# Optimization experiments

Measured on AMD Instinct MI355X. Metric: run time of the kernel, lower is better.

## Reference

```python
import jax, jax.numpy as jnp
import numpy as np

N = 100000
E = 1000000
H = 128
DF = 64
TOTAL_GENES = 20000
NUM_PERTS = 5000


def setup_inputs() -> dict:
    key = jax.random.key(0)
    ks = jax.random.split(key, 32)
    d_in1 = DF + H  # all_feat=True: concat raw feats with gene embedding

    def g(k, shape, scale=0.05):
        return jax.random.normal(k, shape, dtype=jnp.float32) * scale

    inp = {
        'x': jax.random.normal(ks[0], (N, DF), dtype=jnp.float32),
        'edge_index': jax.random.randint(ks[1], (2, E), 0, N),
        'edge_attr': jax.random.normal(ks[2], (E, 1), dtype=jnp.float32),
        'pert': jax.random.randint(ks[3], (N,), 0, NUM_PERTS),
        'ctrl': jax.random.normal(ks[4], (N, 1), dtype=jnp.float32),
        'pos': jax.random.randint(ks[5], (N,), 0, TOTAL_GENES),
        # learned parameters
        'gene_table': g(ks[6], (TOTAL_GENES, H), 1.0),
        'pert_table': g(ks[7], (NUM_PERTS, H), 1.0),
        'W1': g(ks[8], (d_in1, H)), 'a_src1': g(ks[9], (H,)), 'a_dst1': g(ks[10], (H,)), 'b1': g(ks[11], (H,)),
        'Wl1': g(ks[12], (d_in1, H)), 'bl1': g(ks[13], (H,)),
        'W2': g(ks[14], (H, H)), 'a_src2': g(ks[15], (H,)), 'a_dst2': g(ks[16], (H,)), 'b2': g(ks[17], (H,)),
        'Wl2': g(ks[18], (H, H)), 'bl2': g(ks[19], (H,)),
        'Wm1': g(ks[20], (2 * H + 1, H // 2)), 'bm1': g(ks[21], (H // 2,)),
        'Wm2': g(ks[22], (H // 2, 1)), 'bm2': g(ks[23], (1,)),
    }
    return inp


def gat_conv(x, src, dst, W, a_src, a_dst, b, n_nodes):
    # PyG GATConv, heads=1, concat=False, negative_slope=0.2, add_self_loops
    h = x @ W                         # [N, H]
    asrc = h @ a_src                  # [N]
    adst = h @ a_dst                  # [N]
    loop = jnp.arange(n_nodes)
    s = jnp.concatenate([src, loop])  # [E+N]
    d = jnp.concatenate([dst, loop])
    e = jax.nn.leaky_relu(asrc[s] + adst[d], negative_slope=0.2)
    m = jax.ops.segment_max(e, d, num_segments=n_nodes)
    ex = jnp.exp(e - m[d])
    denom = jax.ops.segment_sum(ex, d, num_segments=n_nodes)
    alpha = ex / (denom[d] + 1e-16)
    out = jax.ops.segment_sum(h[s] * alpha[:, None], d, num_segments=n_nodes)
    return out + b


def _forward(x, edge_attr, ctrl, gene_table, pert_table,
             W1, a_src1, a_dst1, b1, Wl1, bl1,
             W2, a_src2, a_dst2, b2, Wl2, bl2,
             Wm1, bm1, Wm2, bm2,
             edge_index, pert, pos):
    src, dst = edge_index[0], edge_index[1]
    # gene embedding with max_norm=True (rows renormed to norm <= 1.0)
    pe = gene_table[pos]
    nrm = jnp.linalg.norm(pe, axis=-1, keepdims=True)
    pe = jnp.where(nrm > 1.0, pe / (nrm + 1e-7), pe)
    h = jnp.concatenate([x, pe], axis=1)            # [N, DF+H]
    h = gat_conv(h, src, dst, W1, a_src1, a_dst1, b1, x.shape[0]) + h @ Wl1 + bl1
    h = jax.nn.relu(h)
    h = gat_conv(h, src, dst, W2, a_src2, a_dst2, b2, x.shape[0]) + h @ Wl2 + bl2
    z = jnp.concatenate([h, ctrl, pert_table[pert]], axis=1)  # [N, 2H+1]
    z = jax.nn.relu(z @ Wm1 + bm1)
    z = jax.nn.relu(z @ Wm2 + bm2)
    return z.squeeze(1)


def reference(x, edge_index, edge_attr, pert, ctrl, pos,
              gene_table, pert_table,
              W1, a_src1, a_dst1, b1, Wl1, bl1,
              W2, a_src2, a_dst2, b2, Wl2, bl2,
              Wm1, bm1, Wm2, bm2):
    return _forward(x, edge_attr, ctrl, gene_table, pert_table,
                    W1, a_src1, a_dst1, b1, Wl1, bl1,
                    W2, a_src2, a_dst2, b2, Wl2, bl2,
                    Wm1, bm1, Wm2, bm2,
                    edge_index, pert, pos)
```

## Files before the change

### kernel.cpp

```cpp
#include <hip/hip_runtime.h>
#include <hip/hip_bf16.h>

typedef __bf16 bf16;
typedef __bf16 bf16x8 __attribute__((ext_vector_type(8)));
typedef __bf16 bf16x4 __attribute__((ext_vector_type(4)));
typedef __bf16 bf16x2 __attribute__((ext_vector_type(2)));
typedef float f32x4 __attribute__((ext_vector_type(4)));

#define CAP 48

__device__ __forceinline__ float b2f(bf16 v) { return (float)v; }
__device__ __forceinline__ bf16 f2b(float v) { return (bf16)v; }

__device__ __forceinline__ float leaky(float x) { return fmaxf(x, 0.2f * x); }

__device__ __forceinline__ bf16x8 zero8() {
    bf16x8 v;
    #pragma unroll
    for (int j = 0; j < 8; ++j) v[j] = (bf16)0.0f;
    return v;
}

__device__ __forceinline__ void swizzle_one(const float* __restrict__ W, bf16* __restrict__ dst,
                                            int f, int NT, int Kreal, int C) {
    int kb = f / (NT * 64);
    int rem = f % (NT * 64);
    int nt = rem / 64;
    int ln = rem % 64;
    int q = ln >> 4, m = ln & 15;
    int c = nt * 16 + m;
    bf16x8 v;
    #pragma unroll
    for (int j = 0; j < 8; ++j) {
        int k = kb * 32 + q * 8 + j;
        v[j] = (k < Kreal) ? f2b(W[k * C + c]) : (bf16)0.0f;
    }
    *reinterpret_cast<bf16x8*>(dst + f * 8) = v;
}

__global__ void scatter_kernel(const int* __restrict__ e_src, const int* __restrict__ e_dst,
                               int* __restrict__ cnt, int* __restrict__ colidx, int e,
                               const float* __restrict__ W1, const float* __restrict__ Wl1,
                               const float* __restrict__ W2, const float* __restrict__ Wl2,
                               const float* __restrict__ Wm1,
                               bf16* __restrict__ w1s, bf16* __restrict__ wl1s,
                               bf16* __restrict__ w2s, bf16* __restrict__ wl2s,
                               bf16* __restrict__ wm1s) {
    int bid = blockIdx.x;
    if (bid < 49) {
        int g = bid * blockDim.x + threadIdx.x;
        if (g < 3072)        swizzle_one(W1,  w1s,  g,          8, 192, 128);
        else if (g < 6144)   swizzle_one(Wl1, wl1s, g - 3072,   8, 192, 128);
        else if (g < 8192)   swizzle_one(W2,  w2s,  g - 6144,   8, 128, 128);
        else if (g < 10240)  swizzle_one(Wl2, wl2s, g - 8192,   8, 128, 128);
        else if (g < 12544)  swizzle_one(Wm1, wm1s, g - 10240,  4, 257,  64);
        return;
    }
    int i = (bid - 49) * blockDim.x + threadIdx.x;
    if (i < e) {
        int d = __builtin_nontemporal_load(e_dst + i);
        int s = __builtin_nontemporal_load(e_src + i);
        int k = atomicAdd(&cnt[d], 1);
        if (k < CAP) __builtin_nontemporal_store(s, colidx + d * CAP + k);
    }
}

template <int KB>
__global__ __launch_bounds__(256) void gemm_l1_kernel(
    const float* __restrict__ x,
    const float* __restrict__ gene_table,
    const int* __restrict__ pos,
    const bf16* __restrict__ Wg, const bf16* __restrict__ Wl,
    const float* __restrict__ bias_l,
    bf16* __restrict__ outg, bf16* __restrict__ outl, int ldo, int nrows,
    const float* __restrict__ attn_s, const float* __restrict__ attn_d,
    float* __restrict__ asrc, float* __restrict__ adst) {
    const int NTT = 8;
    __shared__ bf16 sH[64][200];
    __shared__ float sA[64][2];
    int tid = threadIdx.x;

    {
        int rsub = tid >> 5, l32 = tid & 31;
        #pragma unroll
        for (int rr = 0; rr < 8; ++rr) {
            int rloc = rr * 8 + rsub;
            long long row = (long long)blockIdx.x * 64 + rloc;
            if (row < nrows) {
                const float* g = gene_table + (long long)pos[row] * 128;
                float4 p = reinterpret_cast<const float4*>(g)[l32];
                float ss = p.x * p.x + p.y * p.y + p.z * p.z + p.w * p.w;
                #pragma unroll
                for (int o = 16; o; o >>= 1) ss += __shfl_xor(ss, o, 32);
                float nrm = sqrtf(ss);
                float sc = nrm > 1.0f ? 1.0f / (nrm + 1e-7f) : 1.0f;
                float2 xv = reinterpret_cast<const float2*>(x + row * 64)[l32];
                sH[rloc][2 * l32]     = f2b(xv.x);
                sH[rloc][2 * l32 + 1] = f2b(xv.y);
                sH[rloc][64 + 4 * l32 + 0] = f2b(p.x * sc);
                sH[rloc][64 + 4 * l32 + 1] = f2b(p.y * sc);
                sH[rloc][64 + 4 * l32 + 2] = f2b(p.z * sc);
                sH[rloc][64 + 4 * l32 + 3] = f2b(p.w * sc);
            } else {
                sH[rloc][2 * l32]     = (bf16)0.0f;
                sH[rloc][2 * l32 + 1] = (bf16)0.0f;
                sH[rloc][64 + 4 * l32 + 0] = (bf16)0.0f;
                sH[rloc][64 + 4 * l32 + 1] = (bf16)0.0f;
                sH[rloc][64 + 4 * l32 + 2] = (bf16)0.0f;
                sH[rloc][64 + 4 * l32 + 3] = (bf16)0.0f;
            }
        }
    }
    __syncthreads();

    int wave = tid >> 6, lane = tid & 63;
    int q = lane >> 4, m = lane & 15;
    int nt0 = (wave & 1) * 4;
    int r0loc = (wave >> 1) * 32 + m;
    long long row_base = (long long)blockIdx.x * 64 + (wave >> 1) * 32;
    long long r0 = row_base + m;
    long long r1 = row_base + 16 + m;

    f32x4 accg[2][4], accl[2][4];
    #pragma unroll
    for (int t = 0; t < 2; ++t)
        #pragma unroll
        for (int nt = 0; nt < 4; ++nt) {
            f32x4 z = {0.f, 0.f, 0.f, 0.f};
            accg[t][nt] = z; accl[t][nt] = z;
        }

    #pragma unroll
    for (int kb = 0; kb < KB; ++kb) {
        bf16x8 b0 = *reinterpret_cast<const bf16x8*>(&sH[r0loc][kb * 32 + q * 8]);
        bf16x8 b1 = *reinterpret_cast<const bf16x8*>(&sH[r0loc + 16][kb * 32 + q * 8]);
        #pragma unroll
        for (int nt = 0; nt < 4; ++nt) {
            bf16x8 wg = *reinterpret_cast<const bf16x8*>(Wg + ((kb * NTT + nt0 + nt) * 64 + lane) * 8);
            bf16x8 wl = *reinterpret_cast<const bf16x8*>(Wl + ((kb * NTT + nt0 + nt) * 64 + lane) * 8);
            accg[0][nt] = __builtin_amdgcn_mfma_f32_16x16x32_bf16(wg, b0, accg[0][nt], 0, 0, 0);
            accg[1][nt] = __builtin_amdgcn_mfma_f32_16x16x32_bf16(wg, b1, accg[1][nt], 0, 0, 0);
            accl[0][nt] = __builtin_amdgcn_mfma_f32_16x16x32_bf16(wl, b0, accl[0][nt], 0, 0, 0);
            accl[1][nt] = __builtin_amdgcn_mfma_f32_16x16x32_bf16(wl, b1, accl[1][nt], 0, 0, 0);
        }
    }
    #pragma unroll
    for (int t = 0; t < 2; ++t) {
        long long row = t ? r1 : r0;
        if (row < nrows) {
            #pragma unroll
            for (int nt = 0; nt < 4; ++nt) {
                int c0 = (nt0 + nt) * 16 + q * 4;
                bf16x4 og, ol;
                #pragma unroll
                for (int r = 0; r < 4; ++r) {
                    og[r] = f2b(accg[t][nt][r]);
                    ol[r] = f2b(accl[t][nt][r] + bias_l[c0 + r]);
                }
                *reinterpret_cast<bf16x4*>(outg + row * ldo + c0) = og;
                *reinterpret_cast<bf16x4*>(outl + row * ldo + c0) = ol;
            }
        }
    }
    float svt[2], dvt[2];
    #pragma unroll
    for (int t = 0; t < 2; ++t) {
        float sv = 0.f, dv = 0.f;
        #pragma unroll
        for (int nt = 0; nt < 4; ++nt) {
            int c0 = (nt0 + nt) * 16 + q * 4;
            #pragma unroll
            for (int r = 0; r < 4; ++r) {
                float v = accg[t][nt][r];
                sv = fmaf(v, attn_s[c0 + r], sv);
                dv = fmaf(v, attn_d[c0 + r], dv);
            }
        }
        sv += __shfl_xor(sv, 16); sv += __shfl_xor(sv, 32);
        dv += __shfl_xor(dv, 16); dv += __shfl_xor(dv, 32);
        svt[t] = sv; dvt[t] = dv;
        if ((wave & 1) == 0 && q == 0) {
            int rloc = (wave >> 1) * 32 + t * 16 + m;
            sA[rloc][0] = sv; sA[rloc][1] = dv;
        }
    }
    __syncthreads();
    #pragma unroll
    for (int t = 0; t < 2; ++t) {
        long long row = t ? r1 : r0;
        if ((wave & 1) == 1 && q == 0 && row < nrows) {
            int rloc = (wave >> 1) * 32 + t * 16 + m;
            asrc[row] = svt[t] + sA[rloc][0];
            adst[row] = dvt[t] + sA[rloc][1];
        }
    }
}

template <int KB>
__global__ __launch_bounds__(256) void gemm_dual_kernel(
    const bf16* __restrict__ A, int lda,
    const bf16* __restrict__ Wg, const bf16* __restrict__ Wl,
    const float* __restrict__ bias_l,
    bf16* __restrict__ outg, bf16* __restrict__ outl, int ldo, int nrows,
    const float* __restrict__ attn_s, const float* __restrict__ attn_d,
    float* __restrict__ asrc, float* __restrict__ adst) {
    const int NTT = 8;
    __shared__ float sA[64][2];
    int tid = threadIdx.x;
    int wave = tid >> 6, lane = tid & 63;
    int q = lane >> 4, m = lane & 15;
    int nt0 = (wave & 1) * 4;
    long long row_base = (long long)blockIdx.x * 64 + (wave >> 1) * 32;
    long long r0 = row_base + m;
    long long r1 = row_base + 16 + m;
    bool v0 = r0 < nrows, v1 = r1 < nrows;

    f32x4 accg[2][4], accl[2][4];
    #pragma unroll
    for (int t = 0; t < 2; ++t)
        #pragma unroll
        for (int nt = 0; nt < 4; ++nt) {
            f32x4 z = {0.f, 0.f, 0.f, 0.f};
            accg[t][nt] = z; accl[t][nt] = z;
        }

    bf16x8 b0 = v0 ? *reinterpret_cast<const bf16x8*>(A + r0 * lda + q * 8) : zero8();
    bf16x8 b1 = v1 ? *reinterpret_cast<const bf16x8*>(A + r1 * lda + q * 8) : zero8();
    #pragma unroll
    for (int kb = 0; kb < KB; ++kb) {
        bf16x8 nb0, nb1;
        if (kb + 1 < KB) {
            nb0 = v0 ? *reinterpret_cast<const bf16x8*>(A + r0 * lda + (kb + 1) * 32 + q * 8) : zero8();
            nb1 = v1 ? *reinterpret_cast<const bf16x8*>(A + r1 * lda + (kb + 1) * 32 + q * 8) : zero8();
        }
        #pragma unroll
        for (int nt = 0; nt < 4; ++nt) {
            bf16x8 wg = *reinterpret_cast<const bf16x8*>(Wg + ((kb * NTT + nt0 + nt) * 64 + lane) * 8);
            bf16x8 wl = *reinterpret_cast<const bf16x8*>(Wl + ((kb * NTT + nt0 + nt) * 64 + lane) * 8);
            accg[0][nt] = __builtin_amdgcn_mfma_f32_16x16x32_bf16(wg, b0, accg[0][nt], 0, 0, 0);
            accg[1][nt] = __builtin_amdgcn_mfma_f32_16x16x32_bf16(wg, b1, accg[1][nt], 0, 0, 0);
            accl[0][nt] = __builtin_amdgcn_mfma_f32_16x16x32_bf16(wl, b0, accl[0][nt], 0, 0, 0);
            accl[1][nt] = __builtin_amdgcn_mfma_f32_16x16x32_bf16(wl, b1, accl[1][nt], 0, 0, 0);
        }
        b0 = nb0; b1 = nb1;
    }
    #pragma unroll
    for (int t = 0; t < 2; ++t) {
        long long row = t ? r1 : r0;
        if (row < nrows) {
            #pragma unroll
            for (int nt = 0; nt < 4; ++nt) {
                int c0 = (nt0 + nt) * 16 + q * 4;
                bf16x4 og, ol;
                #pragma unroll
                for (int r = 0; r < 4; ++r) {
                    og[r] = f2b(accg[t][nt][r]);
                    ol[r] = f2b(accl[t][nt][r] + bias_l[c0 + r]);
                }
                *reinterpret_cast<bf16x4*>(outg + row * ldo + c0) = og;
                *reinterpret_cast<bf16x4*>(outl + row * ldo + c0) = ol;
            }
        }
    }
    float svt[2], dvt[2];
    #pragma unroll
    for (int t = 0; t < 2; ++t) {
        float sv = 0.f, dv = 0.f;
        #pragma unroll
        for (int nt = 0; nt < 4; ++nt) {
            int c0 = (nt0 + nt) * 16 + q * 4;
            #pragma unroll
            for (int r = 0; r < 4; ++r) {
                float v = accg[t][nt][r];
                sv = fmaf(v, attn_s[c0 + r], sv);
                dv = fmaf(v, attn_d[c0 + r], dv);
            }
        }
        sv += __shfl_xor(sv, 16); sv += __shfl_xor(sv, 32);
        dv += __shfl_xor(dv, 16); dv += __shfl_xor(dv, 32);
        svt[t] = sv; dvt[t] = dv;
        if ((wave & 1) == 0 && q == 0) {
            int rloc = (wave >> 1) * 32 + t * 16 + m;
            sA[rloc][0] = sv; sA[rloc][1] = dv;
        }
    }
    __syncthreads();
    #pragma unroll
    for (int t = 0; t < 2; ++t) {
        long long row = t ? r1 : r0;
        if ((wave & 1) == 1 && q == 0 && row < nrows) {
            int rloc = (wave >> 1) * 32 + t * 16 + m;
            asrc[row] = svt[t] + sA[rloc][0];
            adst[row] = dvt[t] + sA[rloc][1];
        }
    }
}

template <int KB, int NT>
__global__ __launch_bounds__(256) void gemm_mlp_kernel(
    const bf16* __restrict__ A, int lda,
    const bf16* __restrict__ Wsw,
    const float* __restrict__ bias, int nrows,
    const float* __restrict__ Wm2, const float* __restrict__ bm2,
    float* __restrict__ out_final) {
    int tid = threadIdx.x;
    int wave = tid >> 6, lane = tid & 63;
    int q = lane >> 4, m = lane & 15;
    long long row_base = (long long)blockIdx.x * 128 + wave * 32;
    long long r0 = row_base + m;
    long long r1 = row_base + 16 + m;
    bool v0 = r0 < nrows, v1 = r1 < nrows;

    f32x4 acc[2][NT];
    #pragma unroll
    for (int t = 0; t < 2; ++t)
        #pragma unroll
        for (int nt = 0; nt < NT; ++nt) {
            f32x4 z = {0.f, 0.f, 0.f, 0.f};
            acc[t][nt] = z;
        }

    bf16x8 b0 = v0 ? *reinterpret_cast<const bf16x8*>(A + r0 * lda + q * 8) : zero8();
    bf16x8 b1 = v1 ? *reinterpret_cast<const bf16x8*>(A + r1 * lda + q * 8) : zero8();
    #pragma unroll
    for (int kb = 0; kb < KB; ++kb) {
        bf16x8 nb0, nb1;
        if (kb + 1 < KB) {
            nb0 = v0 ? *reinterpret_cast<const bf16x8*>(A + r0 * lda + (kb + 1) * 32 + q * 8) : zero8();
            nb1 = v1 ? *reinterpret_cast<const bf16x8*>(A + r1 * lda + (kb + 1) * 32 + q * 8) : zero8();
        }
        #pragma unroll
        for (int nt = 0; nt < NT; ++nt) {
            bf16x8 w = *reinterpret_cast<const bf16x8*>(Wsw + ((kb * NT + nt) * 64 + lane) * 8);
            acc[0][nt] = __builtin_amdgcn_mfma_f32_16x16x32_bf16(w, b0, acc[0][nt], 0, 0, 0);
            acc[1][nt] = __builtin_amdgcn_mfma_f32_16x16x32_bf16(w, b1, acc[1][nt], 0, 0, 0);
        }
        b0 = nb0; b1 = nb1;
    }
    #pragma unroll
    for (int t = 0; t < 2; ++t) {
        float sv = 0.f;
        #pragma unroll
        for (int nt = 0; nt < NT; ++nt) {
            int c0 = nt * 16 + q * 4;
            #pragma unroll
            for (int r = 0; r < 4; ++r) {
                float v = fmaxf(acc[t][nt][r] + bias[c0 + r], 0.0f);
                sv = fmaf(v, Wm2[c0 + r], sv);
            }
        }
        sv += __shfl_xor(sv, 16); sv += __shfl_xor(sv, 32);
        long long row = t ? r1 : r0;
        if (q == 0 && row < nrows) out_final[row] = fmaxf(sv + bm2[0], 0.0f);
    }
}

__global__ void gat_edge_kernel(const int* __restrict__ cnt, const int* __restrict__ colidx,
                                const float* __restrict__ asrc, const float* __restrict__ adst,
                                const bf16* __restrict__ hgat, const bf16* __restrict__ hlin,
                                const float* __restrict__ b_gat, int relu,
                                bf16* __restrict__ out, int ldo, int n,
                                const float* __restrict__ ctrl,
                                const float* __restrict__ pert_table,
                                const int* __restrict__ pert) {
    int d = blockIdx.x * 8 + (threadIdx.x >> 5);
    int lane = threadIdx.x & 31;
    if (d >= n) return;
    float ad = adst[d];
    float e_self = leaky(asrc[d] + ad);
    int cn = cnt[d]; if (cn > CAP) cn = CAP;
    bool val0 = lane < cn;
    bool val1 = lane + 32 < cn;
    int sj0 = val0 ? colidx[d * CAP + lane] : d;
    int sj1 = val1 ? colidx[d * CAP + 32 + lane] : d;
    float ej0 = val0 ? leaky(asrc[sj0] + ad) : -1e30f;
    float ej1 = val1 ? leaky(asrc[sj1] + ad) : -1e30f;
    float mx = fmaxf(ej0, ej1);
    #pragma unroll
    for (int o = 16; o; o >>= 1) mx = fmaxf(mx, __shfl_xor(mx, o, 32));
    mx = fmaxf(mx, e_self);
    float wj0 = val0 ? __expf(ej0 - mx) : 0.0f;
    float wj1 = val1 ? __expf(ej1 - mx) : 0.0f;
    float ws = __expf(e_self - mx);
    float sm = wj0 + wj1;
    #pragma unroll
    for (int o = 16; o; o >>= 1) sm += __shfl_xor(sm, o, 32);
    float den = sm + ws;
    bf16x4 hl = *reinterpret_cast<const bf16x4*>(hlin + (long long)d * 128 + 4 * lane);
    float4 bg = *reinterpret_cast<const float4*>(b_gat + 4 * lane);
    bf16x4 hd = *reinterpret_cast<const bf16x4*>(hgat + (long long)d * 128 + 4 * lane);
    float acc0 = ws * b2f(hd[0]), acc1 = ws * b2f(hd[1]);
    float acc2 = ws * b2f(hd[2]), acc3 = ws * b2f(hd[3]);
    int c1 = cn < 32 ? cn : 32;
    for (int j = 0; j < c1; j += 4) {
        int s0 = __shfl(sj0, j, 32), s1 = __shfl(sj0, j + 1, 32);
        int s2 = __shfl(sj0, j + 2, 32), s3 = __shfl(sj0, j + 3, 32);
        float w0 = __shfl(wj0, j, 32), w1 = __shfl(wj0, j + 1, 32);
        float w2 = __shfl(wj0, j + 2, 32), w3 = __shfl(wj0, j + 3, 32);
        bf16x4 h0v = *reinterpret_cast<const bf16x4*>(hgat + (long long)s0 * 128 + 4 * lane);
        bf16x4 h1v = *reinterpret_cast<const bf16x4*>(hgat + (long long)s1 * 128 + 4 * lane);
        bf16x4 h2v = *reinterpret_cast<const bf16x4*>(hgat + (long long)s2 * 128 + 4 * lane);
        bf16x4 h3v = *reinterpret_cast<const bf16x4*>(hgat + (long long)s3 * 128 + 4 * lane);
        acc0 = fmaf(w0, b2f(h0v[0]), acc0); acc1 = fmaf(w0, b2f(h0v[1]), acc1);
        acc2 = fmaf(w0, b2f(h0v[2]), acc2); acc3 = fmaf(w0, b2f(h0v[3]), acc3);
        acc0 = fmaf(w1, b2f(h1v[0]), acc0); acc1 = fmaf(w1, b2f(h1v[1]), acc1);
        acc2 = fmaf(w1, b2f(h1v[2]), acc2); acc3 = fmaf(w1, b2f(h1v[3]), acc3);
        acc0 = fmaf(w2, b2f(h2v[0]), acc0); acc1 = fmaf(w2, b2f(h2v[1]), acc1);
        acc2 = fmaf(w2, b2f(h2v[2]), acc2); acc3 = fmaf(w2, b2f(h2v[3]), acc3);
        acc0 = fmaf(w3, b2f(h3v[0]), acc0); acc1 = fmaf(w3, b2f(h3v[1]), acc1);
        acc2 = fmaf(w3, b2f(h3v[2]), acc2); acc3 = fmaf(w3, b2f(h3v[3]), acc3);
    }
    for (int j = 32; j < cn; j += 4) {
        int s0 = __shfl(sj1, j - 32, 32), s1 = __shfl(sj1, j - 31, 32);
        int s2 = __shfl(sj1, j - 30, 32), s3 = __shfl(sj1, j - 29, 32);
        float w0 = __shfl(wj1, j - 32, 32), w1 = __shfl(wj1, j - 31, 32);
        float w2 = __shfl(wj1, j - 30, 32), w3 = __shfl(wj1, j - 29, 32);
        bf16x4 h0v = *reinterpret_cast<const bf16x4*>(hgat + (long long)s0 * 128 + 4 * lane);
        bf16x4 h1v = *reinterpret_cast<const bf16x4*>(hgat + (long long)s1 * 128 + 4 * lane);
        bf16x4 h2v = *reinterpret_cast<const bf16x4*>(hgat + (long long)s2 * 128 + 4 * lane);
        bf16x4 h3v = *reinterpret_cast<const bf16x4*>(hgat + (long long)s3 * 128 + 4 * lane);
        acc0 = fmaf(w0, b2f(h0v[0]), acc0); acc1 = fmaf(w0, b2f(h0v[1]), acc1);
        acc2 = fmaf(w0, b2f(h0v[2]), acc2); acc3 = fmaf(w0, b2f(h0v[3]), acc3);
        acc0 = fmaf(w1, b2f(h1v[0]), acc0); acc1 = fmaf(w1, b2f(h1v[1]), acc1);
        acc2 = fmaf(w1, b2f(h1v[2]), acc2); acc3 = fmaf(w1, b2f(h1v[3]), acc3);
        acc0 = fmaf(w2, b2f(h2v[0]), acc0); acc1 = fmaf(w2, b2f(h2v[1]), acc1);
        acc2 = fmaf(w2, b2f(h2v[2]), acc2); acc3 = fmaf(w2, b2f(h2v[3]), acc3);
        acc0 = fmaf(w3, b2f(h3v[0]), acc0); acc1 = fmaf(w3, b2f(h3v[1]), acc1);
        acc2 = fmaf(w3, b2f(h3v[2]), acc2); acc3 = fmaf(w3, b2f(h3v[3]), acc3);
    }
    float inv = 1.0f / den;
    float o0 = acc0 * inv + bg.x + b2f(hl[0]);
    float o1 = acc1 * inv + bg.y + b2f(hl[1]);
    float o2 = acc2 * inv + bg.z + b2f(hl[2]);
    float o3 = acc3 * inv + bg.w + b2f(hl[3]);
    if (relu) {
        o0 = fmaxf(o0, 0.0f); o1 = fmaxf(o1, 0.0f);
        o2 = fmaxf(o2, 0.0f); o3 = fmaxf(o3, 0.0f);
    }
    bf16* orow = out + (long long)d * ldo;
    bf16x4 ov; ov[0] = f2b(o0); ov[1] = f2b(o1); ov[2] = f2b(o2); ov[3] = f2b(o3);
    *reinterpret_cast<bf16x4*>(orow + 4 * lane) = ov;
    if (pert) {
        const float* p = pert_table + (long long)pert[d] * 128;
        if (lane == 0) orow[128] = f2b(ctrl[d]);
        orow[129 + lane] = f2b(p[lane]);
        orow[161 + lane] = f2b(p[32 + lane]);
        orow[193 + lane] = f2b(p[64 + lane]);
        orow[225 + lane] = f2b(p[96 + lane]);
        if (lane < 31) orow[257 + lane] = (bf16)0.0f;
    }
}

extern "C" void kernel_launch(void* const* d_in, const int* in_sizes, int n_in,
                              void* d_out, int out_size, void* d_ws, size_t ws_size,
                              hipStream_t stream) {
    const int N = in_sizes[0] / 64;
    const int E = in_sizes[1] / 2;

    const float* x          = (const float*)d_in[0];
    const int*   ei         = (const int*)d_in[1];
    const int*   e_src      = ei;
    const int*   e_dst      = ei + E;
    const int*   pert       = (const int*)d_in[3];
    const float* ctrl       = (const float*)d_in[4];
    const int*   pos        = (const int*)d_in[5];
    const float* gene_table = (const float*)d_in[6];
    const float* pert_table = (const float*)d_in[7];
    const float* W1   = (const float*)d_in[8];
    const float* a_s1 = (const float*)d_in[9];
    const float* a_d1 = (const float*)d_in[10];
    const float* b1   = (const float*)d_in[11];
    const float* Wl1  = (const float*)d_in[12];
    const float* bl1  = (const float*)d_in[13];
    const float* W2   = (const float*)d_in[14];
    const float* a_s2 = (const float*)d_in[15];
    const float* a_d2 = (const float*)d_in[16];
    const float* b2   = (const float*)d_in[17];
    const float* Wl2  = (const float*)d_in[18];
    const float* bl2  = (const float*)d_in[19];
    const float* Wm1  = (const float*)d_in[20];
    const float* bm1  = (const float*)d_in[21];
    const float* Wm2  = (const float*)d_in[22];
    const float* bm2  = (const float*)d_in[23];

    char* ws = (char*)d_ws;
    size_t off = 0;
    auto alloc = [&](size_t bytes) {
        char* p = ws + off;
        off = (off + bytes + 255) & ~(size_t)255;
        return p;
    };
    bf16* hgat   = (bf16*)alloc((size_t)N * 128 * 2);
    bf16* hlin   = (bf16*)alloc((size_t)N * 128 * 2);
    bf16* zregion= (bf16*)alloc((size_t)N * 192 * 2);
    bf16* h1     = (bf16*)alloc((size_t)N * 128 * 2);
    bf16* zbuf   = zregion;
    float* asrc  = (float*)alloc((size_t)N * 4);
    float* adst  = (float*)alloc((size_t)N * 4);
    int* cnt     = (int*)alloc((size_t)N * 4);
    int* colidx  = (int*)alloc((size_t)N * CAP * 4);
    bf16* w1s    = (bf16*)alloc((size_t)3072 * 8 * 2);
    bf16* wl1s   = (bf16*)alloc((size_t)3072 * 8 * 2);
    bf16* w2s    = (bf16*)alloc((size_t)2048 * 8 * 2);
    bf16* wl2s   = (bf16*)alloc((size_t)2048 * 8 * 2);
    bf16* wm1s   = (bf16*)alloc((size_t)2304 * 8 * 2);
    (void)ws_size; (void)n_in; (void)out_size;

    float* out = (float*)d_out;

    const int NBSC = (E + 255) / 256;
    const int NBG64 = (N + 63) / 64;
    const int NBG128 = (N + 127) / 128;
    dim3 blk(256);
    dim3 gridWave((N + 7) / 8);

    hipMemsetAsync(cnt, 0, (size_t)N * 4, stream);
    hipLaunchKernelGGL(scatter_kernel, dim3(49 + NBSC), blk, 0, stream,
                       e_src, e_dst, cnt, colidx, E,
                       W1, Wl1, W2, Wl2, Wm1, w1s, wl1s, w2s, wl2s, wm1s);
    hipLaunchKernelGGL((gemm_l1_kernel<6>), dim3(NBG64), blk, 0, stream,
                       x, gene_table, pos, w1s, wl1s, bl1, hgat, hlin, 128, N,
                       a_s1, a_d1, asrc, adst);
    hipLaunchKernelGGL(gat_edge_kernel, gridWave, blk, 0, stream,
                       cnt, colidx, asrc, adst, hgat, hlin, b1, 1, h1, 128, N,
                       (const float*)nullptr, (const float*)nullptr, (const int*)nullptr);
    hipLaunchKernelGGL((gemm_dual_kernel<4>), dim3(NBG64), blk, 0, stream,
                       h1, 128, w2s, wl2s, bl2, hgat, hlin, 128, N,
                       a_s2, a_d2, asrc, adst);
    hipLaunchKernelGGL(gat_edge_kernel, gridWave, blk, 0, stream,
                       cnt, colidx, asrc, adst, hgat, hlin, b2, 0, zbuf, 288, N,
                       ctrl, pert_table, pert);
    hipLaunchKernelGGL((gemm_mlp_kernel<9, 4>), dim3(NBG128), blk, 0, stream,
                       zbuf, 288, wm1s, bm1, N, Wm2, bm2, out);
}
```

Baseline: 428.1 us.

## Precompute gene-row norm scales in prep kernel and load L1 GEMM operands directly

Adds a per-gene-table-row scale computation to the preprocessing kernel, interleaving it with the edge scatter and weight swizzle blocks. The layer-1 GEMM then drops its LDS staging and block barrier. Each lane reads x and gene-table fragments straight from global memory, applies the precomputed scale, and prefetches the next k-block's fragment while the MFMAs run. This removes the per-node norm reduction and the shared-memory round trip, at the cost of extra work over all 20000 table rows and less coalesced, more redundant global loads across waves.

```diff
diff --git a/kernel.cpp b/kernel.cpp
--- a/kernel.cpp
+++ b/kernel.cpp
@@ -38,17 +38,32 @@
     *reinterpret_cast<bf16x8*>(dst + f * 8) = v;
 }
 
-__global__ void scatter_kernel(const int* __restrict__ e_src, const int* __restrict__ e_dst,
-                               int* __restrict__ cnt, int* __restrict__ colidx, int e,
-                               const float* __restrict__ W1, const float* __restrict__ Wl1,
-                               const float* __restrict__ W2, const float* __restrict__ Wl2,
-                               const float* __restrict__ Wm1,
-                               bf16* __restrict__ w1s, bf16* __restrict__ wl1s,
-                               bf16* __restrict__ w2s, bf16* __restrict__ wl2s,
-                               bf16* __restrict__ wm1s) {
-    int bid = blockIdx.x;
-    if (bid < 49) {
-        int g = bid * blockDim.x + threadIdx.x;
+__global__ void prep_kernel(const float* __restrict__ gene_table, int tg,
+                            const float* __restrict__ W1, const float* __restrict__ Wl1,
+                            const float* __restrict__ W2, const float* __restrict__ Wl2,
+                            const float* __restrict__ Wm1,
+                            bf16* __restrict__ w1s, bf16* __restrict__ wl1s,
+                            bf16* __restrict__ w2s, bf16* __restrict__ wl2s,
+                            bf16* __restrict__ wm1s, float* __restrict__ gscale,
+                            const int* __restrict__ e_src, const int* __restrict__ e_dst,
+                            int* __restrict__ cnt, int* __restrict__ colidx,
+                            int e, int nbsc, int nboth) {
+    int g5 = blockIdx.x / 5, r5 = blockIdx.x % 5;
+    if (r5 == 0) {
+        if (g5 >= nbsc) return;
+        int i = g5 * blockDim.x + threadIdx.x;
+        if (i < e) {
+            int d = __builtin_nontemporal_load(e_dst + i);
+            int s = __builtin_nontemporal_load(e_src + i);
+            int k = atomicAdd(&cnt[d], 1);
+            if (k < CAP) __builtin_nontemporal_store(s, colidx + d * CAP + k);
+        }
+        return;
+    }
+    int ob = g5 * 4 + (r5 - 1);
+    if (ob >= nboth) return;
+    if (ob < 49) {
+        int g = ob * blockDim.x + threadIdx.x;
         if (g < 3072)        swizzle_one(W1,  w1s,  g,          8, 192, 128);
         else if (g < 6144)   swizzle_one(Wl1, wl1s, g - 3072,   8, 192, 128);
         else if (g < 8192)   swizzle_one(W2,  w2s,  g - 6144,   8, 128, 128);
@@ -56,13 +71,38 @@
         else if (g < 12544)  swizzle_one(Wm1, wm1s, g - 10240,  4, 257,  64);
         return;
     }
-    int i = (bid - 49) * blockDim.x + threadIdx.x;
-    if (i < e) {
-        int d = __builtin_nontemporal_load(e_dst + i);
-        int s = __builtin_nontemporal_load(e_src + i);
-        int k = atomicAdd(&cnt[d], 1);
-        if (k < CAP) __builtin_nontemporal_store(s, colidx + d * CAP + k);
-    }
+    int t = (ob - 49) * 8 + (threadIdx.x >> 5);
+    int l = threadIdx.x & 31;
+    if (t >= tg) return;
+    const float* g = gene_table + (long long)t * 128;
+    float4 p = reinterpret_cast<const float4*>(g)[l];
+    float ss = p.x * p.x + p.y * p.y + p.z * p.z + p.w * p.w;
+    #pragma unroll
+    for (int o = 16; o; o >>= 1) ss += __shfl_xor(ss, o);
+    float nrm = sqrtf(ss);
+    float sc = nrm > 1.0f ? 1.0f / (nrm + 1e-7f) : 1.0f;
+    if (l == 0) gscale[t] = sc;
+}
+
+__device__ __forceinline__ bf16x8 l1_frag(const float* __restrict__ xr,
+                                          const float* __restrict__ gr,
+                                          float sc, int kb, int q, bool valid) {
+    if (!valid) return zero8();
+    bf16x8 v;
+    if (kb < 2) {
+        int k0 = kb * 32 + q * 8;
+        float4 a = *reinterpret_cast<const float4*>(xr + k0);
+        float4 b = *reinterpret_cast<const float4*>(xr + k0 + 4);
+        v[0] = f2b(a.x); v[1] = f2b(a.y); v[2] = f2b(a.z); v[3] = f2b(a.w);
+        v[4] = f2b(b.x); v[5] = f2b(b.y); v[6] = f2b(b.z); v[7] = f2b(b.w);
+    } else {
+        int k0 = kb * 32 + q * 8 - 64;
+        float4 a = *reinterpret_cast<const float4*>(gr + k0);
+        float4 b = *reinterpret_cast<const float4*>(gr + k0 + 4);
+        v[0] = f2b(a.x * sc); v[1] = f2b(a.y * sc); v[2] = f2b(a.z * sc); v[3] = f2b(a.w * sc);
+        v[4] = f2b(b.x * sc); v[5] = f2b(b.y * sc); v[6] = f2b(b.z * sc); v[7] = f2b(b.w * sc);
+    }
+    return v;
 }
 
 template <int KB>
@@ -70,56 +110,31 @@
     const float* __restrict__ x,
     const float* __restrict__ gene_table,
     const int* __restrict__ pos,
+    const float* __restrict__ gscale,
     const bf16* __restrict__ Wg, const bf16* __restrict__ Wl,
     const float* __restrict__ bias_l,
     bf16* __restrict__ outg, bf16* __restrict__ outl, int ldo, int nrows,
     const float* __restrict__ attn_s, const float* __restrict__ attn_d,
     float* __restrict__ asrc, float* __restrict__ adst) {
     const int NTT = 8;
-    __shared__ bf16 sH[64][200];
     __shared__ float sA[64][2];
     int tid = threadIdx.x;
-
-    {
-        int rsub = tid >> 5, l32 = tid & 31;
-        #pragma unroll
-        for (int rr = 0; rr < 8; ++rr) {
-            int rloc = rr * 8 + rsub;
-            long long row = (long long)blockIdx.x * 64 + rloc;
-            if (row < nrows) {
-                const float* g = gene_table + (long long)pos[row] * 128;
-                float4 p = reinterpret_cast<const float4*>(g)[l32];
-                float ss = p.x * p.x + p.y * p.y + p.z * p.z + p.w * p.w;
-                #pragma unroll
-                for (int o = 16; o; o >>= 1) ss += __shfl_xor(ss, o, 32);
-                float nrm = sqrtf(ss);
-                float sc = nrm > 1.0f ? 1.0f / (nrm + 1e-7f) : 1.0f;
-                float2 xv = reinterpret_cast<const float2*>(x + row * 64)[l32];
-                sH[rloc][2 * l32]     = f2b(xv.x);
-                sH[rloc][2 * l32 + 1] = f2b(xv.y);
-                sH[rloc][64 + 4 * l32 + 0] = f2b(p.x * sc);
-                sH[rloc][64 + 4 * l32 + 1] = f2b(p.y * sc);
-                sH[rloc][64 + 4 * l32 + 2] = f2b(p.z * sc);
-                sH[rloc][64 + 4 * l32 + 3] = f2b(p.w * sc);
-            } else {
-                sH[rloc][2 * l32]     = (bf16)0.0f;
-                sH[rloc][2 * l32 + 1] = (bf16)0.0f;
-                sH[rloc][64 + 4 * l32 + 0] = (bf16)0.0f;
-                sH[rloc][64 + 4 * l32 + 1] = (bf16)0.0f;
-                sH[rloc][64 + 4 * l32 + 2] = (bf16)0.0f;
-                sH[rloc][64 + 4 * l32 + 3] = (bf16)0.0f;
-            }
-        }
-    }
-    __syncthreads();
-
     int wave = tid >> 6, lane = tid & 63;
     int q = lane >> 4, m = lane & 15;
     int nt0 = (wave & 1) * 4;
-    int r0loc = (wave >> 1) * 32 + m;
     long long row_base = (long long)blockIdx.x * 64 + (wave >> 1) * 32;
     long long r0 = row_base + m;
     long long r1 = row_base + 16 + m;
+    bool v0 = r0 < nrows, v1 = r1 < nrows;
+
+    const float* xr0 = x + r0 * 64;
+    const float* xr1 = x + r1 * 64;
+    int pt0 = v0 ? pos[r0] : 0;
+    int pt1 = v1 ? pos[r1] : 0;
+    const float* gr0 = gene_table + (long long)pt0 * 128;
+    const float* gr1 = gene_table + (long long)pt1 * 128;
+    float sc0 = v0 ? gscale[pt0] : 0.0f;
+    float sc1 = v1 ? gscale[pt1] : 0.0f;
 
     f32x4 accg[2][4], accl[2][4];
     #pragma unroll
@@ -130,10 +145,15 @@
             accg[t][nt] = z; accl[t][nt] = z;
         }
 
+    bf16x8 b0 = l1_frag(xr0, gr0, sc0, 0, q, v0);
+    bf16x8 b1 = l1_frag(xr1, gr1, sc1, 0, q, v1);
     #pragma unroll
     for (int kb = 0; kb < KB; ++kb) {
-        bf16x8 b0 = *reinterpret_cast<const bf16x8*>(&sH[r0loc][kb * 32 + q * 8]);
-        bf16x8 b1 = *reinterpret_cast<const bf16x8*>(&sH[r0loc + 16][kb * 32 + q * 8]);
+        bf16x8 nb0, nb1;
+        if (kb + 1 < KB) {
+            nb0 = l1_frag(xr0, gr0, sc0, kb + 1, q, v0);
+            nb1 = l1_frag(xr1, gr1, sc1, kb + 1, q, v1);
+        }
         #pragma unroll
         for (int nt = 0; nt < 4; ++nt) {
             bf16x8 wg = *reinterpret_cast<const bf16x8*>(Wg + ((kb * NTT + nt0 + nt) * 64 + lane) * 8);
@@ -143,6 +163,7 @@
             accl[0][nt] = __builtin_amdgcn_mfma_f32_16x16x32_bf16(wl, b0, accl[0][nt], 0, 0, 0);
             accl[1][nt] = __builtin_amdgcn_mfma_f32_16x16x32_bf16(wl, b1, accl[1][nt], 0, 0, 0);
         }
+        b0 = nb0; b1 = nb1;
     }
     #pragma unroll
     for (int t = 0; t < 2; ++t) {
@@ -456,6 +477,7 @@
                               hipStream_t stream) {
     const int N = in_sizes[0] / 64;
     const int E = in_sizes[1] / 2;
+    const int TG = in_sizes[6] / 128;
 
     const float* x          = (const float*)d_in[0];
     const int*   ei         = (const int*)d_in[1];
@@ -504,22 +526,27 @@
     bf16* w2s    = (bf16*)alloc((size_t)2048 * 8 * 2);
     bf16* wl2s   = (bf16*)alloc((size_t)2048 * 8 * 2);
     bf16* wm1s   = (bf16*)alloc((size_t)2304 * 8 * 2);
+    float* gscale= (float*)alloc((size_t)TG * 4);
     (void)ws_size; (void)n_in; (void)out_size;
 
     float* out = (float*)d_out;
 
     const int NBSC = (E + 255) / 256;
+    const int NBOTH = 49 + (TG + 7) / 8;
+    const int NG5 = (NBSC > (NBOTH + 3) / 4) ? NBSC : (NBOTH + 3) / 4;
+    const int NBPREP = NG5 * 5;
     const int NBG64 = (N + 63) / 64;
     const int NBG128 = (N + 127) / 128;
     dim3 blk(256);
     dim3 gridWave((N + 7) / 8);
 
     hipMemsetAsync(cnt, 0, (size_t)N * 4, stream);
-    hipLaunchKernelGGL(scatter_kernel, dim3(49 + NBSC), blk, 0, stream,
-                       e_src, e_dst, cnt, colidx, E,
-                       W1, Wl1, W2, Wl2, Wm1, w1s, wl1s, w2s, wl2s, wm1s);
+    hipLaunchKernelGGL(prep_kernel, dim3(NBPREP), blk, 0, stream,
+                       gene_table, TG, W1, Wl1, W2, Wl2, Wm1,
+                       w1s, wl1s, w2s, wl2s, wm1s, gscale,
+                       e_src, e_dst, cnt, colidx, E, NBSC, NBOTH);
     hipLaunchKernelGGL((gemm_l1_kernel<6>), dim3(NBG64), blk, 0, stream,
-                       x, gene_table, pos, w1s, wl1s, bl1, hgat, hlin, 128, N,
+                       x, gene_table, pos, gscale, w1s, wl1s, bl1, hgat, hlin, 128, N,
                        a_s1, a_d1, asrc, adst);
     hipLaunchKernelGGL(gat_edge_kernel, gridWave, blk, 0, stream,
                        cnt, colidx, asrc, adst, hgat, hlin, b1, 1, h1, 128, N,
```

After: 422.3 us. About the same (-1.4%).
